# Kernel tuning notes

Hardware: AMD Instinct MI355X
Metric: run time of the kernel (lower is better)

## Reference

```python
import jax, jax.numpy as jnp
import numpy as np

K = 32          # num_sets (experts)
D_IN = 10       # input_size
D_H = 20        # hidden_size
D_OUT = 1       # output_size
B = 262144      # batch


def setup_inputs() -> dict:
    key = jax.random.key(0)
    ks = jax.random.split(key, 6)
    # Kaiming-uniform-ish init scale like torch Linear defaults
    s1 = 1.0 / np.sqrt(D_IN)
    s2 = 1.0 / np.sqrt(D_H)
    return {
        "input_data": jax.random.normal(ks[0], (B, D_IN), dtype=jnp.float32),
        "W1": jax.random.uniform(ks[1], (K, D_H, D_IN), jnp.float32, -s1, s1),
        "b1": jax.random.uniform(ks[2], (K, D_H), jnp.float32, -s1, s1),
        "W2": jax.random.uniform(ks[3], (K, D_OUT, D_H), jnp.float32, -s2, s2),
        "b2": jax.random.uniform(ks[4], (K, D_OUT), jnp.float32, -s2, s2),
        "prototypes": jax.random.normal(ks[5], (K, D_IN), dtype=jnp.float32),
    }


def reference(input_data, W1, b1, W2, b2, prototypes):
    # All K tiny experts as one batched GEMM: [B,K,H]
    h = jax.nn.relu(jnp.einsum("bi,khi->bkh", input_data, W1) + b1[None])
    preds = jnp.einsum("bkh,koh->bko", h, W2) + b2[None]          # [B,K,O]
    # Distance-based softmax gating over experts
    diff = input_data[:, None, :] - prototypes[None, :, :]        # [B,K,D]
    dist = jnp.sqrt(jnp.sum(diff * diff, axis=2))                 # [B,K]
    attn = jax.nn.softmax(-dist, axis=1)                          # [B,K]
    return jnp.sum(preds * attn[:, :, None], axis=1)              # [B,O]
```

## Files before the change

### kernel.cpp

```cpp
#include <hip/hip_runtime.h>


#define KX 32
#define DIN 10
#define DH 20

typedef short bf16x8 __attribute__((ext_vector_type(8)));
typedef float f32x16 __attribute__((ext_vector_type(16)));

#define ZERO16 {0.f,0.f,0.f,0.f, 0.f,0.f,0.f,0.f, 0.f,0.f,0.f,0.f, 0.f,0.f,0.f,0.f}

__device__ inline unsigned short f2bf(float f) {
    unsigned int u = __float_as_uint(f);
    unsigned int r = u + 0x7fffu + ((u >> 16) & 1u);
    return (unsigned short)(r >> 16);
}

union BFU { bf16x8 v; unsigned short s[8]; };

__global__ __launch_bounds__(256, 4) void moe_kernel(
    const float* __restrict__ x,
    const float* __restrict__ W1,
    const float* __restrict__ b1,
    const float* __restrict__ W2,
    const float* __restrict__ b2,
    const float* __restrict__ proto,
    float* __restrict__ out,
    int B)
{
    __shared__ bf16x8 s_af[KX * 64];
    __shared__ float  s_w2[KX * 32];
    __shared__ bf16x8 s_pf[64];
    __shared__ float  s_pn2[32];

    const int tid = threadIdx.x;

    for (int idx = tid; idx < KX * 64; idx += 256) {
        const int e = idx >> 6, l = idx & 63;
        const int m = l & 31, kb = (l >> 5) * 8;
        BFU u;
#pragma unroll
        for (int j = 0; j < 8; ++j) {
            const int kk = kb + j;
            float v = 0.f;
            if (m < DH) {
                if (kk < DIN) v = W1[(e * DH + m) * DIN + kk];
                else if (kk == DIN) v = b1[e * DH + m];
            }
            u.s[j] = f2bf(v);
        }
        s_af[idx] = u.v;
    }
    for (int idx = tid; idx < KX * 32; idx += 256) {
        const int e = idx >> 5, rem = idx & 31;
        const int half = rem >> 4, reg = rem & 15;
        const int hid = (reg & 3) + 8 * (reg >> 2) + 4 * half;
        s_w2[idx] = (hid < DH) ? W2[e * DH + hid] : 0.f;
    }
    if (tid < 64) {
        const int m = tid & 31, kb = (tid >> 5) * 8;
        BFU u;
#pragma unroll
        for (int j = 0; j < 8; ++j) {
            const int kk = kb + j;
            u.s[j] = f2bf(kk < DIN ? proto[m * DIN + kk] : 0.f);
        }
        s_pf[tid] = u.v;
    }
    if (tid < 32) {
        const int half = tid >> 4, reg = tid & 15;
        const int p = (reg & 3) + 8 * (reg >> 2) + 4 * half;
        float s = 0.f;
#pragma unroll
        for (int i = 0; i < DIN; ++i) { const float v = proto[p * DIN + i]; s = fmaf(v, v, s); }
        s_pn2[tid] = s;
    }
    __syncthreads();

    const int lane = tid & 63;
    const int wave = tid >> 6;
    const int half = lane >> 5;
    const int col  = lane & 31;
    const bf16x8 pfrag = s_pf[lane];
    const float* pn2h = s_pn2 + half * 16;
    const float* w2base = s_w2 + half * 16;

    for (int t = 0; t < 2; ++t) {
        const int tileIdx = (blockIdx.x * 4 + wave) * 2 + t;
        const int row = tileIdx * 32 + col;
        const int rr = (row < B) ? row : (B - 1);

        float xe[8];
        const float* xr = x + (size_t)rr * DIN;
        if (half == 0) {
#pragma unroll
            for (int i = 0; i < 4; ++i) {
                const float2 v = *(const float2*)(xr + 2 * i);
                xe[2 * i] = v.x; xe[2 * i + 1] = v.y;
            }
        } else {
            const float2 v = *(const float2*)(xr + 8);
            xe[0] = v.x; xe[1] = v.y; xe[2] = 1.f;
            xe[3] = 0.f; xe[4] = 0.f; xe[5] = 0.f; xe[6] = 0.f; xe[7] = 0.f;
        }
        BFU xu;
#pragma unroll
        for (int j = 0; j < 8; ++j) xu.s[j] = f2bf(xe[j]);
        const bf16x8 xfrag = xu.v;

        float part;
        if (half == 0) {
            part = 0.f;
#pragma unroll
            for (int j = 0; j < 8; ++j) part = fmaf(xe[j], xe[j], part);
        } else {
            part = fmaf(xe[0], xe[0], xe[1] * xe[1]);
        }
        const float xn2 = part + __shfl_xor(part, 32);

        f32x16 zg = ZERO16;
        const f32x16 dotg = __builtin_amdgcn_mfma_f32_32x32x16_bf16(pfrag, xfrag, zg, 0, 0, 0);

        float gate[16];
#pragma unroll
        for (int q = 0; q < 16; ++q) {
            float d2 = fmaf(dotg[q], -2.f, xn2 + pn2h[q]);
            d2 = fmaxf(d2, 0.f);
            gate[q] = __expf(-__fsqrt_rn(d2));
        }

        float accn[16];
#pragma unroll 2
        for (int j = 0; j < 16; ++j) {
            const int elo = (j & 3) + 8 * (j >> 2);
            const int ehi = elo + 4;
            const bf16x8 alo = s_af[elo * 64 + lane];
            const bf16x8 ahi = s_af[ehi * 64 + lane];
            f32x16 z0 = ZERO16, z1 = ZERO16;
            const f32x16 clo = __builtin_amdgcn_mfma_f32_32x32x16_bf16(alo, xfrag, z0, 0, 0, 0);
            const f32x16 chi = __builtin_amdgcn_mfma_f32_32x32x16_bf16(ahi, xfrag, z1, 0, 0, 0);
            const float* w2lo = w2base + elo * 32;
            const float* w2hi = w2base + ehi * 32;
            float pplo = 0.f, pphi = 0.f;
#pragma unroll
            for (int q = 0; q < 16; ++q) {
                pplo = fmaf(fmaxf(clo[q], 0.f), w2lo[q], pplo);
                pphi = fmaf(fmaxf(chi[q], 0.f), w2hi[q], pphi);
            }
            const float plo = pplo + __shfl_xor(pplo, 32);
            const float phi = pphi + __shfl_xor(pphi, 32);
            const float pred = half ? (phi + b2[ehi]) : (plo + b2[elo]);
            accn[j] = gate[j] * pred;
        }

        float nsum = 0.f, dsum = 0.f;
#pragma unroll
        for (int q = 0; q < 16; ++q) { nsum += accn[q]; dsum += gate[q]; }
        nsum += __shfl_xor(nsum, 32);
        dsum += __shfl_xor(dsum, 32);
        if (half == 0 && row < B) out[row] = nsum / dsum;
    }
}

extern "C" void kernel_launch(void* const* d_in, const int* in_sizes, int n_in,
                              void* d_out, int out_size, void* d_ws, size_t ws_size,
                              hipStream_t stream) {
    const float* x     = (const float*)d_in[0];
    const float* W1    = (const float*)d_in[1];
    const float* b1    = (const float*)d_in[2];
    const float* W2    = (const float*)d_in[3];
    const float* b2    = (const float*)d_in[4];
    const float* proto = (const float*)d_in[5];
    float* out = (float*)d_out;

    const int B = out_size;
    const int rows_per_block = 4 * 2 * 32;
    const int grid = (B + rows_per_block - 1) / rows_per_block;
    hipLaunchKernelGGL(moe_kernel, dim3(grid), dim3(256), 0, stream,
                       x, W1, b1, W2, b2, proto, out, B);
}
```

Before: 104.9 us.

## Shrink LDS weight table, one tile per wave, vectorize epilogue, defer shuffles

Packs the W1 fragment table to 40 entries per expert instead of 64, dropping the padded rows to cut LDS use. Raises the occupancy hint to 6 and gives each wave a single 32-row tile, which doubles the grid and the per-block weight staging. The per-expert cross-half shuffles are replaced by pre-exchanging the gate values once and accumulating both halves' predictions locally. b2 is folded into the gate-weighted sum, and the relu/W2 dot product uses packed float2 FMAs. The expert loop is no longer unrolled, which may reduce instruction-level parallelism.

New measurement: 110.4 us. 1.05x slower.

```diff
diff --git a/kernel.cpp b/kernel.cpp
--- a/kernel.cpp
+++ b/kernel.cpp
@@ -7,6 +7,7 @@
 
 typedef short bf16x8 __attribute__((ext_vector_type(8)));
 typedef float f32x16 __attribute__((ext_vector_type(16)));
+typedef float v2f    __attribute__((ext_vector_type(2)));
 
 #define ZERO16 {0.f,0.f,0.f,0.f, 0.f,0.f,0.f,0.f, 0.f,0.f,0.f,0.f, 0.f,0.f,0.f,0.f}
 
@@ -18,7 +19,7 @@
 
 union BFU { bf16x8 v; unsigned short s[8]; };
 
-__global__ __launch_bounds__(256, 4) void moe_kernel(
+__global__ __launch_bounds__(256, 6) void moe_kernel(
     const float* __restrict__ x,
     const float* __restrict__ W1,
     const float* __restrict__ b1,
@@ -28,33 +29,32 @@
     float* __restrict__ out,
     int B)
 {
-    __shared__ bf16x8 s_af[KX * 64];
+    __shared__ bf16x8 s_af[KX * 40];
     __shared__ float  s_w2[KX * 32];
     __shared__ bf16x8 s_pf[64];
     __shared__ float  s_pn2[32];
+    __shared__ float  s_b2c[32];
 
     const int tid = threadIdx.x;
 
-    for (int idx = tid; idx < KX * 64; idx += 256) {
-        const int e = idx >> 6, l = idx & 63;
-        const int m = l & 31, kb = (l >> 5) * 8;
+    for (int idx = tid; idx < KX * 40; idx += 256) {
+        const int e = idx / 40, rem = idx - e * 40;
+        const int hf = rem / 20, m = rem - hf * 20;
         BFU u;
 #pragma unroll
         for (int j = 0; j < 8; ++j) {
-            const int kk = kb + j;
+            const int kk = hf * 8 + j;
             float v = 0.f;
-            if (m < DH) {
-                if (kk < DIN) v = W1[(e * DH + m) * DIN + kk];
-                else if (kk == DIN) v = b1[e * DH + m];
-            }
+            if (kk < DIN) v = W1[(e * DH + m) * DIN + kk];
+            else if (kk == DIN) v = b1[e * DH + m];
             u.s[j] = f2bf(v);
         }
         s_af[idx] = u.v;
     }
     for (int idx = tid; idx < KX * 32; idx += 256) {
         const int e = idx >> 5, rem = idx & 31;
-        const int half = rem >> 4, reg = rem & 15;
-        const int hid = (reg & 3) + 8 * (reg >> 2) + 4 * half;
+        const int hf = rem >> 4, q = rem & 15;
+        const int hid = (q & 3) + 8 * (q >> 2) + 4 * hf;
         s_w2[idx] = (hid < DH) ? W2[e * DH + hid] : 0.f;
     }
     if (tid < 64) {
@@ -68,12 +68,13 @@
         s_pf[tid] = u.v;
     }
     if (tid < 32) {
-        const int half = tid >> 4, reg = tid & 15;
-        const int p = (reg & 3) + 8 * (reg >> 2) + 4 * half;
+        const int hf = tid >> 4, q = tid & 15;
+        const int p = (q & 3) + 8 * (q >> 2) + 4 * hf;
         float s = 0.f;
 #pragma unroll
         for (int i = 0; i < DIN; ++i) { const float v = proto[p * DIN + i]; s = fmaf(v, v, s); }
         s_pn2[tid] = s;
+        s_b2c[tid] = b2[p];
     }
     __syncthreads();
 
@@ -81,85 +82,101 @@
     const int wave = tid >> 6;
     const int half = lane >> 5;
     const int col  = lane & 31;
-    const bf16x8 pfrag = s_pf[lane];
-    const float* pn2h = s_pn2 + half * 16;
-    const float* w2base = s_w2 + half * 16;
 
-    for (int t = 0; t < 2; ++t) {
-        const int tileIdx = (blockIdx.x * 4 + wave) * 2 + t;
-        const int row = tileIdx * 32 + col;
-        const int rr = (row < B) ? row : (B - 1);
+    const int row = (blockIdx.x * 4 + wave) * 32 + col;
+    const int rr = (row < B) ? row : (B - 1);
 
-        float xe[8];
-        const float* xr = x + (size_t)rr * DIN;
-        if (half == 0) {
+    float xe[8];
+    const float* xr = x + (size_t)rr * DIN;
+    if (half == 0) {
 #pragma unroll
-            for (int i = 0; i < 4; ++i) {
-                const float2 v = *(const float2*)(xr + 2 * i);
-                xe[2 * i] = v.x; xe[2 * i + 1] = v.y;
-            }
-        } else {
-            const float2 v = *(const float2*)(xr + 8);
-            xe[0] = v.x; xe[1] = v.y; xe[2] = 1.f;
-            xe[3] = 0.f; xe[4] = 0.f; xe[5] = 0.f; xe[6] = 0.f; xe[7] = 0.f;
+        for (int i = 0; i < 4; ++i) {
+            const float2 v = *(const float2*)(xr + 2 * i);
+            xe[2 * i] = v.x; xe[2 * i + 1] = v.y;
         }
-        BFU xu;
+    } else {
+        const float2 v = *(const float2*)(xr + 8);
+        xe[0] = v.x; xe[1] = v.y; xe[2] = 1.f;
+        xe[3] = 0.f; xe[4] = 0.f; xe[5] = 0.f; xe[6] = 0.f; xe[7] = 0.f;
+    }
+    BFU xu;
 #pragma unroll
-        for (int j = 0; j < 8; ++j) xu.s[j] = f2bf(xe[j]);
-        const bf16x8 xfrag = xu.v;
+    for (int j = 0; j < 8; ++j) xu.s[j] = f2bf(xe[j]);
+    const bf16x8 xfrag = xu.v;
 
-        float part;
-        if (half == 0) {
-            part = 0.f;
+    float part;
+    if (half == 0) {
+        part = 0.f;
 #pragma unroll
-            for (int j = 0; j < 8; ++j) part = fmaf(xe[j], xe[j], part);
-        } else {
-            part = fmaf(xe[0], xe[0], xe[1] * xe[1]);
+        for (int j = 0; j < 8; ++j) part = fmaf(xe[j], xe[j], part);
+    } else {
+        part = fmaf(xe[0], xe[0], xe[1] * xe[1]);
+    }
+    const float xn2 = part + __shfl_xor(part, 32);
+
+    f32x16 zg = ZERO16;
+    const f32x16 dotg = __builtin_amdgcn_mfma_f32_32x32x16_bf16(s_pf[lane], xfrag, zg, 0, 0, 0);
+
+    float gate[16], gx[16];
+    float dsum = 0.f, nsum = 0.f;
+    {
+        const v2f* pn2v = (const v2f*)(s_pn2 + half * 16);
+        const float* b2c = s_b2c + half * 16;
+#pragma unroll
+        for (int i = 0; i < 8; ++i) {
+            v2f dv = v2f{dotg[2 * i], dotg[2 * i + 1]};
+            v2f s2 = pn2v[i] + v2f{xn2, xn2};
+            v2f d2 = __builtin_elementwise_fma(dv, v2f{-2.f, -2.f}, s2);
+            d2 = __builtin_elementwise_max(d2, v2f{0.f, 0.f});
+            const float g0 = __expf(-__fsqrt_rn(d2.x));
+            const float g1 = __expf(-__fsqrt_rn(d2.y));
+            gate[2 * i] = g0; gate[2 * i + 1] = g1;
+            dsum += g0 + g1;
+            nsum = fmaf(g0, b2c[2 * i], nsum);
+            nsum = fmaf(g1, b2c[2 * i + 1], nsum);
         }
-        const float xn2 = part + __shfl_xor(part, 32);
+#pragma unroll
+        for (int q = 0; q < 16; ++q) gx[q] = __shfl_xor(gate[q], 32);
+    }
 
-        f32x16 zg = ZERO16;
-        const f32x16 dotg = __builtin_amdgcn_mfma_f32_32x32x16_bf16(pfrag, xfrag, zg, 0, 0, 0);
+    const int mrow = col;
+#pragma unroll 1
+    for (int j = 0; j < 16; ++j) {
+        const int elo = (j & 3) + 8 * (j >> 2);
+        const int ehi = elo + 4;
 
-        float gate[16];
+        bf16x8 alo = {0, 0, 0, 0, 0, 0, 0, 0};
+        bf16x8 ahi = {0, 0, 0, 0, 0, 0, 0, 0};
+        if (mrow < DH) {
+            alo = s_af[elo * 40 + half * 20 + mrow];
+            ahi = s_af[ehi * 40 + half * 20 + mrow];
+        }
+        f32x16 z0 = ZERO16, z1 = ZERO16;
+        const f32x16 clo = __builtin_amdgcn_mfma_f32_32x32x16_bf16(alo, xfrag, z0, 0, 0, 0);
+        const f32x16 chi = __builtin_amdgcn_mfma_f32_32x32x16_bf16(ahi, xfrag, z1, 0, 0, 0);
+
+        const v2f* w2lo = (const v2f*)(s_w2 + elo * 32 + half * 16);
+        const v2f* w2hi = (const v2f*)(s_w2 + ehi * 32 + half * 16);
+        v2f plov = v2f{0.f, 0.f}, phiv = v2f{0.f, 0.f};
 #pragma unroll
-        for (int q = 0; q < 16; ++q) {
-            float d2 = fmaf(dotg[q], -2.f, xn2 + pn2h[q]);
-            d2 = fmaxf(d2, 0.f);
-            gate[q] = __expf(-__fsqrt_rn(d2));
+        for (int i = 0; i < 8; ++i) {
+            v2f cl = __builtin_elementwise_max(v2f{clo[2 * i], clo[2 * i + 1]}, v2f{0.f, 0.f});
+            v2f ch = __builtin_elementwise_max(v2f{chi[2 * i], chi[2 * i + 1]}, v2f{0.f, 0.f});
+            plov = __builtin_elementwise_fma(cl, w2lo[i], plov);
+            phiv = __builtin_elementwise_fma(ch, w2hi[i], phiv);
         }
+        const float pplo = plov.x + plov.y;
+        const float pphi = phiv.x + phiv.y;
 
-        float accn[16];
-#pragma unroll 2
-        for (int j = 0; j < 16; ++j) {
-            const int elo = (j & 3) + 8 * (j >> 2);
-            const int ehi = elo + 4;
-            const bf16x8 alo = s_af[elo * 64 + lane];
-            const bf16x8 ahi = s_af[ehi * 64 + lane];
-            f32x16 z0 = ZERO16, z1 = ZERO16;
-            const f32x16 clo = __builtin_amdgcn_mfma_f32_32x32x16_bf16(alo, xfrag, z0, 0, 0, 0);
-            const f32x16 chi = __builtin_amdgcn_mfma_f32_32x32x16_bf16(ahi, xfrag, z1, 0, 0, 0);
-            const float* w2lo = w2base + elo * 32;
-            const float* w2hi = w2base + ehi * 32;
-            float pplo = 0.f, pphi = 0.f;
-#pragma unroll
-            for (int q = 0; q < 16; ++q) {
-                pplo = fmaf(fmaxf(clo[q], 0.f), w2lo[q], pplo);
-                pphi = fmaf(fmaxf(chi[q], 0.f), w2hi[q], pphi);
-            }
-            const float plo = pplo + __shfl_xor(pplo, 32);
-            const float phi = pphi + __shfl_xor(pphi, 32);
-            const float pred = half ? (phi + b2[ehi]) : (plo + b2[elo]);
-            accn[j] = gate[j] * pred;
-        }
+        const float p_own = half ? pphi : pplo;
+        const float p_oth = half ? pplo : pphi;
+        nsum = fmaf(gate[j], p_own, nsum);
+        nsum = fmaf(gx[j],   p_oth, nsum);
+    }
 
-        float nsum = 0.f, dsum = 0.f;
-#pragma unroll
-        for (int q = 0; q < 16; ++q) { nsum += accn[q]; dsum += gate[q]; }
-        nsum += __shfl_xor(nsum, 32);
-        dsum += __shfl_xor(dsum, 32);
-        if (half == 0 && row < B) out[row] = nsum / dsum;
-    }
+    nsum += __shfl_xor(nsum, 32);
+    dsum += __shfl_xor(dsum, 32);
+    if (half == 0 && row < B) out[row] = nsum / dsum;
 }
 
 extern "C" void kernel_launch(void* const* d_in, const int* in_sizes, int n_in,
@@ -174,7 +191,7 @@
     float* out = (float*)d_out;
 
     const int B = out_size;
-    const int rows_per_block = 4 * 2 * 32;
+    const int rows_per_block = 4 * 32;
     const int grid = (B + rows_per_block - 1) / rows_per_block;
     hipLaunchKernelGGL(moe_kernel, dim3(grid), dim3(256), 0, stream,
                        x, W1, b1, W2, b2, proto, out, B);
```

## Compact W1 LDS layout, one tile per wave, packed FMA for W2 reduction

Applied to the files above, without the earlier changes.

The shared W1 fragment table shrinks from 64 to 40 entries per expert by dropping the padded rows, and lanes past the hidden size feed zero fragments instead of loading them. Each wave now handles a single 32-row tile rather than looping over two, which doubles the grid. The second-layer reduction uses float4 LDS reads and packed two-wide max/FMA. The aim is lower LDS use, shorter per-block setup, and cheaper ALU work in the inner loop. The cost is that the per-block weight staging is repeated across twice as many blocks.

After: 107.7 us. 2.6% more time.

```diff
diff --git a/kernel.cpp b/kernel.cpp
--- a/kernel.cpp
+++ b/kernel.cpp
@@ -7,6 +7,7 @@
 
 typedef short bf16x8 __attribute__((ext_vector_type(8)));
 typedef float f32x16 __attribute__((ext_vector_type(16)));
+typedef float v2f    __attribute__((ext_vector_type(2)));
 
 #define ZERO16 {0.f,0.f,0.f,0.f, 0.f,0.f,0.f,0.f, 0.f,0.f,0.f,0.f, 0.f,0.f,0.f,0.f}
 
@@ -28,33 +29,31 @@
     float* __restrict__ out,
     int B)
 {
-    __shared__ bf16x8 s_af[KX * 64];
+    __shared__ bf16x8 s_af[KX * 40];
     __shared__ float  s_w2[KX * 32];
     __shared__ bf16x8 s_pf[64];
     __shared__ float  s_pn2[32];
 
     const int tid = threadIdx.x;
 
-    for (int idx = tid; idx < KX * 64; idx += 256) {
-        const int e = idx >> 6, l = idx & 63;
-        const int m = l & 31, kb = (l >> 5) * 8;
+    for (int idx = tid; idx < KX * 40; idx += 256) {
+        const int e = idx / 40, rem = idx - e * 40;
+        const int hf = rem / 20, m = rem - hf * 20;
         BFU u;
 #pragma unroll
         for (int j = 0; j < 8; ++j) {
-            const int kk = kb + j;
+            const int kk = hf * 8 + j;
             float v = 0.f;
-            if (m < DH) {
-                if (kk < DIN) v = W1[(e * DH + m) * DIN + kk];
-                else if (kk == DIN) v = b1[e * DH + m];
-            }
+            if (kk < DIN) v = W1[(e * DH + m) * DIN + kk];
+            else if (kk == DIN) v = b1[e * DH + m];
             u.s[j] = f2bf(v);
         }
         s_af[idx] = u.v;
     }
     for (int idx = tid; idx < KX * 32; idx += 256) {
         const int e = idx >> 5, rem = idx & 31;
-        const int half = rem >> 4, reg = rem & 15;
-        const int hid = (reg & 3) + 8 * (reg >> 2) + 4 * half;
+        const int hf = rem >> 4, q = rem & 15;
+        const int hid = (q & 3) + 8 * (q >> 2) + 4 * hf;
         s_w2[idx] = (hid < DH) ? W2[e * DH + hid] : 0.f;
     }
     if (tid < 64) {
@@ -68,8 +67,8 @@
         s_pf[tid] = u.v;
     }
     if (tid < 32) {
-        const int half = tid >> 4, reg = tid & 15;
-        const int p = (reg & 3) + 8 * (reg >> 2) + 4 * half;
+        const int hf = tid >> 4, q = tid & 15;
+        const int p = (q & 3) + 8 * (q >> 2) + 4 * hf;
         float s = 0.f;
 #pragma unroll
         for (int i = 0; i < DIN; ++i) { const float v = proto[p * DIN + i]; s = fmaf(v, v, s); }
@@ -83,83 +82,96 @@
     const int col  = lane & 31;
     const bf16x8 pfrag = s_pf[lane];
     const float* pn2h = s_pn2 + half * 16;
-    const float* w2base = s_w2 + half * 16;
 
-    for (int t = 0; t < 2; ++t) {
-        const int tileIdx = (blockIdx.x * 4 + wave) * 2 + t;
-        const int row = tileIdx * 32 + col;
-        const int rr = (row < B) ? row : (B - 1);
+    const int row = (blockIdx.x * 4 + wave) * 32 + col;
+    const int rr = (row < B) ? row : (B - 1);
 
-        float xe[8];
-        const float* xr = x + (size_t)rr * DIN;
-        if (half == 0) {
+    float xe[8];
+    const float* xr = x + (size_t)rr * DIN;
+    if (half == 0) {
 #pragma unroll
-            for (int i = 0; i < 4; ++i) {
-                const float2 v = *(const float2*)(xr + 2 * i);
-                xe[2 * i] = v.x; xe[2 * i + 1] = v.y;
-            }
-        } else {
-            const float2 v = *(const float2*)(xr + 8);
-            xe[0] = v.x; xe[1] = v.y; xe[2] = 1.f;
-            xe[3] = 0.f; xe[4] = 0.f; xe[5] = 0.f; xe[6] = 0.f; xe[7] = 0.f;
+        for (int i = 0; i < 4; ++i) {
+            const float2 v = *(const float2*)(xr + 2 * i);
+            xe[2 * i] = v.x; xe[2 * i + 1] = v.y;
         }
-        BFU xu;
+    } else {
+        const float2 v = *(const float2*)(xr + 8);
+        xe[0] = v.x; xe[1] = v.y; xe[2] = 1.f;
+        xe[3] = 0.f; xe[4] = 0.f; xe[5] = 0.f; xe[6] = 0.f; xe[7] = 0.f;
+    }
+    BFU xu;
 #pragma unroll
-        for (int j = 0; j < 8; ++j) xu.s[j] = f2bf(xe[j]);
-        const bf16x8 xfrag = xu.v;
+    for (int j = 0; j < 8; ++j) xu.s[j] = f2bf(xe[j]);
+    const bf16x8 xfrag = xu.v;
 
-        float part;
-        if (half == 0) {
-            part = 0.f;
+    float part;
+    if (half == 0) {
+        part = 0.f;
 #pragma unroll
-            for (int j = 0; j < 8; ++j) part = fmaf(xe[j], xe[j], part);
-        } else {
-            part = fmaf(xe[0], xe[0], xe[1] * xe[1]);
+        for (int j = 0; j < 8; ++j) part = fmaf(xe[j], xe[j], part);
+    } else {
+        part = fmaf(xe[0], xe[0], xe[1] * xe[1]);
+    }
+    const float xn2 = part + __shfl_xor(part, 32);
+
+    f32x16 zg = ZERO16;
+    const f32x16 dotg = __builtin_amdgcn_mfma_f32_32x32x16_bf16(pfrag, xfrag, zg, 0, 0, 0);
+
+    float gate[16];
+#pragma unroll
+    for (int q = 0; q < 16; ++q) {
+        float d2 = fmaf(dotg[q], -2.f, xn2 + pn2h[q]);
+        d2 = fmaxf(d2, 0.f);
+        gate[q] = __expf(-__fsqrt_rn(d2));
+    }
+
+    const int mrow = col;
+    float accn[16];
+#pragma unroll 2
+    for (int j = 0; j < 16; ++j) {
+        const int elo = (j & 3) + 8 * (j >> 2);
+        const int ehi = elo + 4;
+
+        bf16x8 alo = {0, 0, 0, 0, 0, 0, 0, 0};
+        bf16x8 ahi = {0, 0, 0, 0, 0, 0, 0, 0};
+        if (mrow < DH) {
+            alo = s_af[elo * 40 + half * 20 + mrow];
+            ahi = s_af[ehi * 40 + half * 20 + mrow];
         }
-        const float xn2 = part + __shfl_xor(part, 32);
+        f32x16 z0 = ZERO16, z1 = ZERO16;
+        const f32x16 clo = __builtin_amdgcn_mfma_f32_32x32x16_bf16(alo, xfrag, z0, 0, 0, 0);
+        const f32x16 chi = __builtin_amdgcn_mfma_f32_32x32x16_bf16(ahi, xfrag, z1, 0, 0, 0);
 
-        f32x16 zg = ZERO16;
-        const f32x16 dotg = __builtin_amdgcn_mfma_f32_32x32x16_bf16(pfrag, xfrag, zg, 0, 0, 0);
+        const float4* w4lo = (const float4*)(s_w2 + elo * 32 + half * 16);
+        const float4* w4hi = (const float4*)(s_w2 + ehi * 32 + half * 16);
+        v2f plov = v2f{0.f, 0.f}, phiv = v2f{0.f, 0.f};
+#pragma unroll
+        for (int i = 0; i < 4; ++i) {
+            const float4 wl = w4lo[i];
+            const float4 wh = w4hi[i];
+            v2f cl0 = __builtin_elementwise_max(v2f{clo[4 * i + 0], clo[4 * i + 1]}, v2f{0.f, 0.f});
+            v2f cl1 = __builtin_elementwise_max(v2f{clo[4 * i + 2], clo[4 * i + 3]}, v2f{0.f, 0.f});
+            v2f ch0 = __builtin_elementwise_max(v2f{chi[4 * i + 0], chi[4 * i + 1]}, v2f{0.f, 0.f});
+            v2f ch1 = __builtin_elementwise_max(v2f{chi[4 * i + 2], chi[4 * i + 3]}, v2f{0.f, 0.f});
+            plov = __builtin_elementwise_fma(cl0, v2f{wl.x, wl.y}, plov);
+            plov = __builtin_elementwise_fma(cl1, v2f{wl.z, wl.w}, plov);
+            phiv = __builtin_elementwise_fma(ch0, v2f{wh.x, wh.y}, phiv);
+            phiv = __builtin_elementwise_fma(ch1, v2f{wh.z, wh.w}, phiv);
+        }
+        const float pplo = plov.x + plov.y;
+        const float pphi = phiv.x + phiv.y;
+        const float plo = pplo + __shfl_xor(pplo, 32);
+        const float phi = pphi + __shfl_xor(pphi, 32);
+        const float pred = half ? (phi + b2[ehi]) : (plo + b2[elo]);
+        accn[j] = gate[j] * pred;
+    }
 
-        float gate[16];
+    float nsum = 0.f, dsum = 0.f;
 #pragma unroll
-        for (int q = 0; q < 16; ++q) {
-            float d2 = fmaf(dotg[q], -2.f, xn2 + pn2h[q]);
-            d2 = fmaxf(d2, 0.f);
-            gate[q] = __expf(-__fsqrt_rn(d2));
-        }
-
-        float accn[16];
-#pragma unroll 2
-        for (int j = 0; j < 16; ++j) {
-            const int elo = (j & 3) + 8 * (j >> 2);
-            const int ehi = elo + 4;
-            const bf16x8 alo = s_af[elo * 64 + lane];
-            const bf16x8 ahi = s_af[ehi * 64 + lane];
-            f32x16 z0 = ZERO16, z1 = ZERO16;
-            const f32x16 clo = __builtin_amdgcn_mfma_f32_32x32x16_bf16(alo, xfrag, z0, 0, 0, 0);
-            const f32x16 chi = __builtin_amdgcn_mfma_f32_32x32x16_bf16(ahi, xfrag, z1, 0, 0, 0);
-            const float* w2lo = w2base + elo * 32;
-            const float* w2hi = w2base + ehi * 32;
-            float pplo = 0.f, pphi = 0.f;
-#pragma unroll
-            for (int q = 0; q < 16; ++q) {
-                pplo = fmaf(fmaxf(clo[q], 0.f), w2lo[q], pplo);
-                pphi = fmaf(fmaxf(chi[q], 0.f), w2hi[q], pphi);
-            }
-            const float plo = pplo + __shfl_xor(pplo, 32);
-            const float phi = pphi + __shfl_xor(pphi, 32);
-            const float pred = half ? (phi + b2[ehi]) : (plo + b2[elo]);
-            accn[j] = gate[j] * pred;
-        }
-
-        float nsum = 0.f, dsum = 0.f;
-#pragma unroll
-        for (int q = 0; q < 16; ++q) { nsum += accn[q]; dsum += gate[q]; }
-        nsum += __shfl_xor(nsum, 32);
-        dsum += __shfl_xor(dsum, 32);
-        if (half == 0 && row < B) out[row] = nsum / dsum;
-    }
+    for (int q = 0; q < 16; ++q) { nsum += accn[q]; dsum += gate[q]; }
+    nsum += __shfl_xor(nsum, 32);
+    dsum += __shfl_xor(dsum, 32);
+    if (half == 0 && row < B) out[row] = nsum / dsum;
 }
 
 extern "C" void kernel_launch(void* const* d_in, const int* in_sizes, int n_in,
@@ -174,7 +186,7 @@
     float* out = (float*)d_out;
 
     const int B = out_size;
-    const int rows_per_block = 4 * 2 * 32;
+    const int rows_per_block = 4 * 32;
     const int grid = (B + rows_per_block - 1) / rows_per_block;
     hipLaunchKernelGGL(moe_kernel, dim3(grid), dim3(256), 0, stream,
                        x, W1, b1, W2, b2, proto, out, B);
```
